# Performance work log

Hardware: AMD Instinct MI355X
Metric: run time of the kernel (lower is better)

Reference implementation:

```python
import jax, jax.numpy as jnp
import numpy as np

K = 7  # kernel_size (odd)
PAD = K // 2
EPS = 1e-12  # F.normalize eps


def setup_inputs() -> dict:
    key = jax.random.key(0)
    kx, ky = jax.random.split(key)
    B, C, H, W = 4, 256, 256, 256
    x = jax.random.normal(kx, (B, C, H, W), dtype=jnp.float32)
    y = jax.random.normal(ky, (B, C, H, W), dtype=jnp.float32)
    return {"x": x, "y": y}


def _l2_normalize(t):
    # F.normalize(t, p=2, dim=1): divide by channel L2 norm, clamped at eps
    n = jnp.sqrt(jnp.sum(t * t, axis=1, keepdims=True))
    return t / jnp.maximum(n, EPS)


def reference(x, y):
    xn = _l2_normalize(x)
    yn = _l2_normalize(y)
    B, C, H, W = x.shape  # H == W assumed (module mixes h/w in slicing)
    yp = jnp.pad(yn, ((0, 0), (0, 0), (PAD, PAD), (PAD, PAD)))
    # Fixed K*K offset loop (small, static); each term reduces over channels.
    sims = [
        jnp.sum(xn * jax.lax.dynamic_slice(yp, (0, 0, i, j), (B, C, H, W)), axis=1)
        for i in range(K)
        for j in range(K)
    ]
    return jnp.stack(sims, axis=1)  # [B, K*K, H, W]
```

## Files before the change

### kernel.cpp

```cpp
#include <hip/hip_runtime.h>


#define H_ 256
#define W_ 256
#define C_ 256
#define B_ 4
#define TH 16
#define TW 16
#define KCH 32
#define NCHUNK (C_ / KCH)
#define HAL (TH + 6)
#define WAL (TW + 6)
#define PLANE (H_ * W_)

typedef __attribute__((ext_vector_type(8))) short short8;
typedef __attribute__((ext_vector_type(4))) float floatx4;
typedef __attribute__((ext_vector_type(4))) unsigned uint32x4;

__device__ __forceinline__ unsigned bfpair(float a, float b) {
  unsigned ua = __float_as_uint(a), ub = __float_as_uint(b);
  ua = (ua + 0x7FFFu + ((ua >> 16) & 1u)) >> 16;
  ub = (ub + 0x7FFFu + ((ub >> 16) & 1u)) & 0xFFFF0000u;
  return ub | ua;
}

__global__ __launch_bounds__(1024) void ncorr(const float* __restrict__ x,
                                              const float* __restrict__ y,
                                              float* __restrict__ out) {
  __shared__ __align__(16) short Yb[2][HAL * 4 * WAL * 8];
  __shared__ float sxl[TH * TW];
  __shared__ float syl[HAL * WAL];
  float* Ob = (float*)&Yb[0][0];

  const int t = threadIdx.x;

  int id = (blockIdx.z * gridDim.y + blockIdx.y) * gridDim.x + blockIdx.x;
  int sw = (id & 7) * 128 + (id >> 3);
  const int b = sw >> 8;
  const int h0 = ((sw >> 4) & 15) * TH;
  const int w0 = (sw & 15) * TW;

  if (t < HAL * WAL) syl[t] = 0.f;

  const int lane = t & 63;
  const int wv = t >> 6;
  const int q = lane >> 4;
  const int lr = lane & 15;

  const int xbase = ((b * C_ + q * 8) * H_ + (h0 + wv)) * W_ + (w0 + lr);

  const bool yact = (t < 968);
  bool yin = false;
  int ybase = 0, yslot = 0, ypos = 0;
  if (yact) {
    int cg2 = t / 484;
    int r = t - cg2 * 484;
    int hy = r / 22;
    int wy = r - hy * 22;
    int gy = h0 - 3 + hy, gx = w0 - 3 + wy;
    yin = (gy >= 0) && (gy < H_) && (gx >= 0) && (gx < W_);
    ybase = ((b * C_ + cg2 * 16) * H_ + (yin ? gy : 0)) * W_ + (yin ? gx : 0);
    yslot = (hy * 4 + cg2 * 2) * 22 + wy;
    ypos = hy * 22 + wy;
  }
  float sxacc = 0.f, syacc = 0.f;

  floatx4 acc[7][2];
#pragma unroll
  for (int i = 0; i < 7; i++) {
    acc[i][0] = (floatx4){0.f, 0.f, 0.f, 0.f};
    acc[i][1] = (floatx4){0.f, 0.f, 0.f, 0.f};
  }

  const int w2a = lr;
  const int w2b = (lr < 6) ? (16 + lr) : 21;

  float xr[2][8];
  float yr[2][16];
#pragma unroll
  for (int s = 0; s < 2; s++) {
#pragma unroll
    for (int k = 0; k < 16; k++) yr[s][k] = 0.f;
  }

#pragma unroll
  for (int j = 0; j < 8; j++) xr[0][j] = x[xbase + j * PLANE];
  if (yact) {
    if (yin) {
#pragma unroll
      for (int k = 0; k < 16; k++) yr[0][k] = y[ybase + k * PLANE];
    }
    unsigned p[8];
#pragma unroll
    for (int k = 0; k < 8; k++) {
      syacc += yr[0][2 * k] * yr[0][2 * k] + yr[0][2 * k + 1] * yr[0][2 * k + 1];
      p[k] = bfpair(yr[0][2 * k], yr[0][2 * k + 1]);
    }
    uint32x4 v0 = {p[0], p[1], p[2], p[3]};
    uint32x4 v1 = {p[4], p[5], p[6], p[7]};
    *(uint32x4*)&Yb[0][yslot * 8] = v0;
    *(uint32x4*)&Yb[0][(yslot + 22) * 8] = v1;
  }
  __syncthreads();

#pragma unroll
  for (int ch = 0; ch < NCHUNK; ch++) {
    const int cur = ch & 1, nxt = cur ^ 1;
    const int cof = (ch + 1) * KCH * PLANE;
    if (ch < NCHUNK - 1) {
#pragma unroll
      for (int j = 0; j < 8; j++) xr[nxt][j] = x[xbase + cof + j * PLANE];
      if (yact && yin) {
#pragma unroll
        for (int k = 0; k < 16; k++) yr[nxt][k] = y[ybase + cof + k * PLANE];
      }
    }
    uint32x4 av;
#pragma unroll
    for (int k = 0; k < 4; k++) {
      sxacc += xr[cur][2 * k] * xr[cur][2 * k] + xr[cur][2 * k + 1] * xr[cur][2 * k + 1];
      av[k] = bfpair(xr[cur][2 * k], xr[cur][2 * k + 1]);
    }
    short8 A = __builtin_bit_cast(short8, av);
#pragma unroll
    for (int i = 0; i < 7; i++) {
      const int rb = ((wv + i) * 4 + q) * 22;
      short8 B0 = *(const short8*)&Yb[cur][(rb + w2a) * 8];
      acc[i][0] = __builtin_amdgcn_mfma_f32_16x16x32_bf16(A, B0, acc[i][0], 0, 0, 0);
      short8 B1 = *(const short8*)&Yb[cur][(rb + w2b) * 8];
      acc[i][1] = __builtin_amdgcn_mfma_f32_16x16x32_bf16(A, B1, acc[i][1], 0, 0, 0);
    }
    if (ch < NCHUNK - 1 && yact) {
      unsigned p[8];
#pragma unroll
      for (int k = 0; k < 8; k++) {
        syacc += yr[nxt][2 * k] * yr[nxt][2 * k] + yr[nxt][2 * k + 1] * yr[nxt][2 * k + 1];
        p[k] = bfpair(yr[nxt][2 * k], yr[nxt][2 * k + 1]);
      }
      uint32x4 v0 = {p[0], p[1], p[2], p[3]};
      uint32x4 v1 = {p[4], p[5], p[6], p[7]};
      *(uint32x4*)&Yb[nxt][yslot * 8] = v0;
      *(uint32x4*)&Yb[nxt][(yslot + 22) * 8] = v1;
    }
    __syncthreads();
  }

  float xs = sxacc;
  xs += __shfl_xor(xs, 16);
  xs += __shfl_xor(xs, 32);
  if (q == 0) sxl[wv * 16 + lr] = 1.f / fmaxf(sqrtf(xs), 1e-12f);
  if (yact) atomicAdd(&syl[ypos], syacc);
  __syncthreads();
  if (t < HAL * WAL) syl[t] = 1.f / fmaxf(sqrtf(syl[t]), 1e-12f);
  __syncthreads();

#pragma unroll
  for (int i = 0; i < 7; i++) {
#pragma unroll
    for (int nt = 0; nt < 2; nt++) {
      const int n = nt * 16 + lr;
#pragma unroll
      for (int r = 0; r < 4; r++) {
        const int m = q * 4 + r;
        const int j = n - m;
        if (j >= 0 && j < 7) {
          float v = acc[i][nt][r] * sxl[wv * 16 + m] * syl[(wv + i) * 22 + n];
          Ob[(7 * i + j) * 260 + wv * 16 + m] = v;
        }
      }
    }
  }
  __syncthreads();
  for (int idx = t; idx < 49 * 256; idx += 1024) {
    const int chn = idx >> 8;
    const int rem = idx & 255;
    __builtin_nontemporal_store(
        Ob[chn * 260 + rem],
        &out[((b * 49 + chn) * H_ + h0 + (rem >> 4)) * W_ + (w0 + (rem & 15))]);
  }
}

extern "C" void kernel_launch(void* const* d_in, const int* in_sizes, int n_in,
                              void* d_out, int out_size, void* d_ws, size_t ws_size,
                              hipStream_t stream) {
  const float* x = (const float*)d_in[0];
  const float* y = (const float*)d_in[1];
  float* out = (float*)d_out;
  dim3 grid(W_ / TW, H_ / TH, B_);
  ncorr<<<grid, 1024, 0, stream>>>(x, y, out);
}
```

Measured before the change: 741.1 us.

## Deepen global-load prefetch to two chunks ahead and drop nontemporal output stores

Restructures the channel-chunk loop so global loads of x and y are issued two chunks ahead, converting and staging the next chunk after the MFMAs. A sched_barrier pins the loads ahead of the MFMA block. The goal is to hide more HBM latency behind the matrix work. It also swaps nontemporal output stores for plain stores, and in exchange holds more registers live at 1024 threads per block.

```diff
diff --git a/kernel.cpp b/kernel.cpp
--- a/kernel.cpp
+++ b/kernel.cpp
@@ -85,11 +85,27 @@
 
 #pragma unroll
   for (int j = 0; j < 8; j++) xr[0][j] = x[xbase + j * PLANE];
+  if (yact && yin) {
+#pragma unroll
+    for (int k = 0; k < 16; k++) yr[0][k] = y[ybase + k * PLANE];
+  }
+#pragma unroll
+  for (int j = 0; j < 8; j++) xr[1][j] = x[xbase + KCH * PLANE + j * PLANE];
+  if (yact && yin) {
+#pragma unroll
+    for (int k = 0; k < 16; k++) yr[1][k] = y[ybase + KCH * PLANE + k * PLANE];
+  }
+  short8 A_cur, A_next;
+  {
+    uint32x4 av;
+#pragma unroll
+    for (int k = 0; k < 4; k++) {
+      sxacc += xr[0][2 * k] * xr[0][2 * k] + xr[0][2 * k + 1] * xr[0][2 * k + 1];
+      av[k] = bfpair(xr[0][2 * k], xr[0][2 * k + 1]);
+    }
+    A_cur = __builtin_bit_cast(short8, av);
+  }
   if (yact) {
-    if (yin) {
-#pragma unroll
-      for (int k = 0; k < 16; k++) yr[0][k] = y[ybase + k * PLANE];
-    }
     unsigned p[8];
 #pragma unroll
     for (int k = 0; k < 8; k++) {
@@ -104,45 +120,49 @@
   __syncthreads();
 
 #pragma unroll
-  for (int ch = 0; ch < NCHUNK; ch++) {
-    const int cur = ch & 1, nxt = cur ^ 1;
-    const int cof = (ch + 1) * KCH * PLANE;
-    if (ch < NCHUNK - 1) {
-#pragma unroll
-      for (int j = 0; j < 8; j++) xr[nxt][j] = x[xbase + cof + j * PLANE];
+  for (int P = 0; P < NCHUNK; P++) {
+    const int cur = P & 1, nxt = cur ^ 1;
+    if (P + 2 < NCHUNK) {
+      const int cof = (P + 2) * KCH * PLANE;
+#pragma unroll
+      for (int j = 0; j < 8; j++) xr[cur][j] = x[xbase + cof + j * PLANE];
       if (yact && yin) {
 #pragma unroll
-        for (int k = 0; k < 16; k++) yr[nxt][k] = y[ybase + cof + k * PLANE];
-      }
-    }
-    uint32x4 av;
-#pragma unroll
-    for (int k = 0; k < 4; k++) {
-      sxacc += xr[cur][2 * k] * xr[cur][2 * k] + xr[cur][2 * k + 1] * xr[cur][2 * k + 1];
-      av[k] = bfpair(xr[cur][2 * k], xr[cur][2 * k + 1]);
-    }
-    short8 A = __builtin_bit_cast(short8, av);
+        for (int k = 0; k < 16; k++) yr[cur][k] = y[ybase + cof + k * PLANE];
+      }
+    }
+    __builtin_amdgcn_sched_barrier(0);
 #pragma unroll
     for (int i = 0; i < 7; i++) {
       const int rb = ((wv + i) * 4 + q) * 22;
       short8 B0 = *(const short8*)&Yb[cur][(rb + w2a) * 8];
-      acc[i][0] = __builtin_amdgcn_mfma_f32_16x16x32_bf16(A, B0, acc[i][0], 0, 0, 0);
+      acc[i][0] = __builtin_amdgcn_mfma_f32_16x16x32_bf16(A_cur, B0, acc[i][0], 0, 0, 0);
       short8 B1 = *(const short8*)&Yb[cur][(rb + w2b) * 8];
-      acc[i][1] = __builtin_amdgcn_mfma_f32_16x16x32_bf16(A, B1, acc[i][1], 0, 0, 0);
-    }
-    if (ch < NCHUNK - 1 && yact) {
-      unsigned p[8];
-#pragma unroll
-      for (int k = 0; k < 8; k++) {
-        syacc += yr[nxt][2 * k] * yr[nxt][2 * k] + yr[nxt][2 * k + 1] * yr[nxt][2 * k + 1];
-        p[k] = bfpair(yr[nxt][2 * k], yr[nxt][2 * k + 1]);
-      }
-      uint32x4 v0 = {p[0], p[1], p[2], p[3]};
-      uint32x4 v1 = {p[4], p[5], p[6], p[7]};
-      *(uint32x4*)&Yb[nxt][yslot * 8] = v0;
-      *(uint32x4*)&Yb[nxt][(yslot + 22) * 8] = v1;
+      acc[i][1] = __builtin_amdgcn_mfma_f32_16x16x32_bf16(A_cur, B1, acc[i][1], 0, 0, 0);
+    }
+    if (P + 1 < NCHUNK) {
+      uint32x4 av;
+#pragma unroll
+      for (int k = 0; k < 4; k++) {
+        sxacc += xr[nxt][2 * k] * xr[nxt][2 * k] + xr[nxt][2 * k + 1] * xr[nxt][2 * k + 1];
+        av[k] = bfpair(xr[nxt][2 * k], xr[nxt][2 * k + 1]);
+      }
+      A_next = __builtin_bit_cast(short8, av);
+      if (yact) {
+        unsigned p[8];
+#pragma unroll
+        for (int k = 0; k < 8; k++) {
+          syacc += yr[nxt][2 * k] * yr[nxt][2 * k] + yr[nxt][2 * k + 1] * yr[nxt][2 * k + 1];
+          p[k] = bfpair(yr[nxt][2 * k], yr[nxt][2 * k + 1]);
+        }
+        uint32x4 v0 = {p[0], p[1], p[2], p[3]};
+        uint32x4 v1 = {p[4], p[5], p[6], p[7]};
+        *(uint32x4*)&Yb[nxt][yslot * 8] = v0;
+        *(uint32x4*)&Yb[nxt][(yslot + 22) * 8] = v1;
+      }
     }
     __syncthreads();
+    A_cur = A_next;
   }
 
   float xs = sxacc;
@@ -174,9 +194,8 @@
   for (int idx = t; idx < 49 * 256; idx += 1024) {
     const int chn = idx >> 8;
     const int rem = idx & 255;
-    __builtin_nontemporal_store(
-        Ob[chn * 260 + rem],
-        &out[((b * 49 + chn) * H_ + h0 + (rem >> 4)) * W_ + (w0 + (rem & 15))]);
+    out[((b * 49 + chn) * H_ + h0 + (rem >> 4)) * W_ + (w0 + (rem & 15))] =
+        Ob[chn * 260 + rem];
   }
 }
 
```

Result: slower. 796.3 us (+7.4%).
